# Kernel optimization log

Measured on AMD Instinct MI355X. Metric: run time of the kernel, lower is better.

Reference implementation:

```python
import jax, jax.numpy as jnp
import numpy as np


def channel_attention(x):
    # Faithful to torch: proj_key = x.view(B, -1, C) is a memory RESHAPE, not a transpose.
    B, C, H, W = x.shape
    N = H * W
    pq = x.reshape(B, C, N)          # [B, C, N]
    pk = x.reshape(B, N, C)          # [B, N, C] -- reshape, NOT pq transposed
    attn = jax.nn.softmax(jnp.einsum('bcn,bnd->bcd', pq, pk), axis=-1)  # [B, C, C]
    out = jnp.einsum('bcd,bdn->bcn', attn, pq).reshape(B, C, H, W)
    return out + x


def positional_attention(x):
    B, C, H, W = x.shape
    N = H * W
    pk = x.reshape(B, C, N)                                  # [B, C, N]
    # proj_query = pk transposed -> attn[b, n, m] over spatial positions
    attn = jax.nn.softmax(jnp.einsum('bcn,bcm->bnm', pk, pk), axis=-1)  # [B, N, N]
    # out = bmm(pk, attn^T): out[b, c, m] = sum_n pk[b, c, n] * attn[b, m, n]
    out = jnp.einsum('bcn,bmn->bcm', pk, attn).reshape(B, C, H, W)
    return out + x


def setup_inputs() -> dict:
    key = jax.random.key(0)
    x = jax.random.normal(key, (4, 512, 64, 64), dtype=jnp.float32)
    return {"x": x}


def reference(x):
    x_ca = channel_attention(x)
    x_pa = positional_attention(x_ca)
    return x_pa
```

## Files before the change

kernel.cpp:

```cpp
#include <hip/hip_runtime.h>

#define BATCH 4
#define CH 512
#define NSP 4096

typedef __attribute__((ext_vector_type(8))) short bfrag8;
typedef __attribute__((ext_vector_type(4))) float f32x4;
typedef unsigned short u16;

#define AS1 __attribute__((address_space(1)))
#define AS3 __attribute__((address_space(3)))
__device__ __forceinline__ void gload16(const void* g, void* l) {
    __builtin_amdgcn_global_load_lds((const AS1 void*)g, (AS3 void*)l, 16, 0, 0);
}

__device__ __forceinline__ void split_bf16(float y, u16& h, u16& l) {
    unsigned int u = __float_as_uint(y);
    h = (u16)(u >> 16);
    float r = y - __uint_as_float(((unsigned int)h) << 16);
    l = (u16)(__float_as_uint(r) >> 16);
}
__device__ __forceinline__ float join_bf16(u16 h, u16 l) {
    return __uint_as_float(((unsigned int)h) << 16) + __uint_as_float(((unsigned int)l) << 16);
}

__global__ __launch_bounds__(256) void k_prep_cn(const float* __restrict__ X,
                                                 u16* __restrict__ XHi,
                                                 u16* __restrict__ XLo,
                                                 u16* __restrict__ XT1hi,
                                                 u16* __restrict__ XT1lo) {
    __shared__ unsigned int t[64][65];
    const size_t boff = (size_t)blockIdx.z * CH * NSP;
    const int c0 = blockIdx.y * 64, n0 = blockIdx.x * 64;
    const int r = threadIdx.x >> 4, col4 = (threadIdx.x & 15) * 4;
#pragma unroll
    for (int it = 0; it < 4; it++) {
        int rl = r + it * 16;
        float4 v = *(const float4*)(X + boff + (size_t)(c0 + rl) * NSP + n0 + col4);
        ushort4 h, l;
        split_bf16(v.x, h.x, l.x);
        split_bf16(v.y, h.y, l.y);
        split_bf16(v.z, h.z, l.z);
        split_bf16(v.w, h.w, l.w);
        *(ushort4*)(XHi + boff + (size_t)(c0 + rl) * NSP + n0 + col4) = h;
        *(ushort4*)(XLo + boff + (size_t)(c0 + rl) * NSP + n0 + col4) = l;
        t[rl][col4 + 0] = ((unsigned int)h.x << 16) | l.x;
        t[rl][col4 + 1] = ((unsigned int)h.y << 16) | l.y;
        t[rl][col4 + 2] = ((unsigned int)h.z << 16) | l.z;
        t[rl][col4 + 3] = ((unsigned int)h.w << 16) | l.w;
    }
    __syncthreads();
#pragma unroll
    for (int it = 0; it < 4; it++) {
        int cl = r + it * 16;
        unsigned int p0 = t[col4 + 0][cl];
        unsigned int p1 = t[col4 + 1][cl];
        unsigned int p2 = t[col4 + 2][cl];
        unsigned int p3 = t[col4 + 3][cl];
        ushort4 hv, lv;
        hv.x = p0 >> 16; hv.y = p1 >> 16; hv.z = p2 >> 16; hv.w = p3 >> 16;
        lv.x = p0 & 0xffff; lv.y = p1 & 0xffff; lv.z = p2 & 0xffff; lv.w = p3 & 0xffff;
        *(ushort4*)(XT1hi + boff + (size_t)(n0 + cl) * CH + c0 + col4) = hv;
        *(ushort4*)(XT1lo + boff + (size_t)(n0 + cl) * CH + c0 + col4) = lv;
    }
}

__global__ __launch_bounds__(256) void k_prep_nc(const float* __restrict__ X,
                                                 u16* __restrict__ XT2hi,
                                                 u16* __restrict__ XT2lo) {
    __shared__ unsigned int t[64][65];
    const size_t boff = (size_t)blockIdx.z * CH * NSP;
    const int n0 = blockIdx.x * 64, d0 = blockIdx.y * 64;
    const int r = threadIdx.x >> 4, col4 = (threadIdx.x & 15) * 4;
#pragma unroll
    for (int it = 0; it < 4; it++) {
        int rl = r + it * 16;
        float4 v = *(const float4*)(X + boff + (size_t)(n0 + rl) * CH + d0 + col4);
        ushort4 h, l;
        split_bf16(v.x, h.x, l.x);
        split_bf16(v.y, h.y, l.y);
        split_bf16(v.z, h.z, l.z);
        split_bf16(v.w, h.w, l.w);
        t[rl][col4 + 0] = ((unsigned int)h.x << 16) | l.x;
        t[rl][col4 + 1] = ((unsigned int)h.y << 16) | l.y;
        t[rl][col4 + 2] = ((unsigned int)h.z << 16) | l.z;
        t[rl][col4 + 3] = ((unsigned int)h.w << 16) | l.w;
    }
    __syncthreads();
#pragma unroll
    for (int it = 0; it < 4; it++) {
        int cl = r + it * 16;
        unsigned int p0 = t[col4 + 0][cl];
        unsigned int p1 = t[col4 + 1][cl];
        unsigned int p2 = t[col4 + 2][cl];
        unsigned int p3 = t[col4 + 3][cl];
        ushort4 hv, lv;
        hv.x = p0 >> 16; hv.y = p1 >> 16; hv.z = p2 >> 16; hv.w = p3 >> 16;
        lv.x = p0 & 0xffff; lv.y = p1 & 0xffff; lv.z = p2 & 0xffff; lv.w = p3 & 0xffff;
        *(ushort4*)(XT2hi + boff + (size_t)(d0 + cl) * NSP + n0 + col4) = hv;
        *(ushort4*)(XT2lo + boff + (size_t)(d0 + cl) * NSP + n0 + col4) = lv;
    }
}

__global__ __launch_bounds__(256, 2) void k1_mfma(const u16* __restrict__ XHi,
                                                  const u16* __restrict__ XLo,
                                                  const u16* __restrict__ XT2hi,
                                                  const u16* __restrict__ XT2lo,
                                                  float* __restrict__ Pk) {
    __shared__ __align__(16) char smem[32768];
    char* Ahi = smem;
    char* Alo = smem + 8192;
    char* Bhi = smem + 16384;
    char* Blo = smem + 24576;
    const int bid = blockIdx.x;
    const int xcd = bid & 7;
    const int i1 = bid >> 3;
    const int group = xcd * 4 + (i1 >> 4);
    const int b = group >> 3, kz = group & 7;
    const int tile = i1 & 15;
    const int c0 = (tile >> 2) * 128, d0 = (tile & 3) * 128;
    const size_t boff = (size_t)b * CH * NSP;
    const int tid = threadIdx.x, lane = tid & 63, w = tid >> 6;
    const int wr = w >> 1, wc = w & 1;
    const int rl = lane >> 2;
    const int cb = (lane & 3) * 8;
    f32x4 acc[4][4];
#pragma unroll
    for (int i = 0; i < 4; i++)
#pragma unroll
        for (int j = 0; j < 4; j++) acc[i][j] = (f32x4){0.f, 0.f, 0.f, 0.f};

    const int kbeg = kz * 512, kend = kbeg + 512;
    for (int k0 = kbeg; k0 < kend; k0 += 32) {
#pragma unroll
        for (int s = 0; s < 2; s++) {
            int idx = w * 2 + s;
            int row = 16 * idx + rl;
            gload16(XHi + boff + (size_t)(c0 + row) * NSP + k0 + cb, Ahi + idx * 1024);
            gload16(XLo + boff + (size_t)(c0 + row) * NSP + k0 + cb, Alo + idx * 1024);
            gload16(XT2hi + boff + (size_t)(d0 + row) * NSP + k0 + cb, Bhi + idx * 1024);
            gload16(XT2lo + boff + (size_t)(d0 + row) * NSP + k0 + cb, Blo + idx * 1024);
        }
        __syncthreads();
        bfrag8 ah[4], al[4], bh[4], bl[4];
        const int q16 = (lane >> 4) * 16;
        const int l15 = (lane & 15);
#pragma unroll
        for (int i = 0; i < 4; i++) {
            int offa = (wr * 64 + i * 16 + l15) * 64 + q16;
            ah[i] = *(const bfrag8*)(Ahi + offa);
            al[i] = *(const bfrag8*)(Alo + offa);
            int offb = (wc * 64 + i * 16 + l15) * 64 + q16;
            bh[i] = *(const bfrag8*)(Bhi + offb);
            bl[i] = *(const bfrag8*)(Blo + offb);
        }
#pragma unroll
        for (int i = 0; i < 4; i++)
#pragma unroll
            for (int j = 0; j < 4; j++) {
                acc[i][j] = __builtin_amdgcn_mfma_f32_16x16x32_bf16(ah[i], bh[j], acc[i][j], 0, 0, 0);
                acc[i][j] = __builtin_amdgcn_mfma_f32_16x16x32_bf16(ah[i], bl[j], acc[i][j], 0, 0, 0);
                acc[i][j] = __builtin_amdgcn_mfma_f32_16x16x32_bf16(al[i], bh[j], acc[i][j], 0, 0, 0);
            }
        __syncthreads();
    }
    float* Lb = Pk + (size_t)kz * BATCH * CH * CH + (size_t)b * CH * CH;
    const int col = lane & 15, qr = (lane >> 4) * 4;
#pragma unroll
    for (int i = 0; i < 4; i++)
#pragma unroll
        for (int j = 0; j < 4; j++)
#pragma unroll
            for (int r = 0; r < 4; r++)
                Lb[(size_t)(c0 + wr * 64 + 16 * i + qr + r) * CH + d0 + wc * 64 + 16 * j + col] =
                    acc[i][j][r];
}

__global__ __launch_bounds__(256) void k_combine8(const float* __restrict__ Pk,
                                                  float* __restrict__ Lg) {
    const size_t MM = (size_t)BATCH * CH * CH;
    size_t i = ((size_t)blockIdx.x * 256 + threadIdx.x) * 4;
    float4 s = *(const float4*)(Pk + i);
#pragma unroll
    for (int z = 1; z < 8; z++) {
        float4 v = *(const float4*)(Pk + z * MM + i);
        s.x += v.x; s.y += v.y; s.z += v.z; s.w += v.w;
    }
    *(float4*)(Lg + i) = s;
}

__global__ __launch_bounds__(256) void k_softmax_pack512(float* __restrict__ Lg) {
    __shared__ float buf[512];
    __shared__ float red[256];
    const int tid = threadIdx.x;
    float* row = Lg + (size_t)blockIdx.x * 512;
    float2 v = *(const float2*)(row + tid * 2);
    buf[tid * 2] = v.x;
    buf[tid * 2 + 1] = v.y;
    red[tid] = fmaxf(v.x, v.y);
    __syncthreads();
    for (int s = 128; s > 0; s >>= 1) {
        if (tid < s) red[tid] = fmaxf(red[tid], red[tid + s]);
        __syncthreads();
    }
    float m = red[0];
    __syncthreads();
    float e0 = __expf(buf[tid * 2] - m), e1 = __expf(buf[tid * 2 + 1] - m);
    buf[tid * 2] = e0;
    buf[tid * 2 + 1] = e1;
    red[tid] = e0 + e1;
    __syncthreads();
    for (int s = 128; s > 0; s >>= 1) {
        if (tid < s) red[tid] += red[tid + s];
        __syncthreads();
    }
    float inv = 1.0f / red[0];
    u16* u = (u16*)row;
    u16 h0, l0, h1, l1;
    split_bf16(buf[tid * 2] * inv, h0, l0);
    split_bf16(buf[tid * 2 + 1] * inv, h1, l1);
    __syncthreads();
    u[tid * 2] = h0;
    u[tid * 2 + 1] = h1;
    u[512 + tid * 2] = l0;
    u[512 + tid * 2 + 1] = l1;
}

__global__ __launch_bounds__(256, 2) void k3_mfma(const u16* __restrict__ Lu,
                                                  const u16* __restrict__ XT1hi,
                                                  const u16* __restrict__ XT1lo,
                                                  const float* __restrict__ X,
                                                  u16* __restrict__ Yhi,
                                                  u16* __restrict__ Ylo,
                                                  u16* __restrict__ YThi,
                                                  u16* __restrict__ YTlo) {
    __shared__ __align__(16) char smem[33280];
    char* Ahi = smem;
    char* Alo = smem + 8192;
    char* Bhi = smem + 16384;
    char* Blo = smem + 24576;
    const int b = blockIdx.z;
    const u16* Au = Lu + (size_t)b * CH * 1024;
    const size_t boff = (size_t)b * CH * NSP;
    const float* Xb = X + boff;
    const int tid = threadIdx.x, lane = tid & 63, w = tid >> 6;
    const int wr = w >> 1, wc = w & 1;
    const int c0 = blockIdx.y * 128, n0 = blockIdx.x * 128;
    const int rl = lane >> 2;
    const int cb = (lane & 3) * 8;
    f32x4 acc[4][4];
#pragma unroll
    for (int i = 0; i < 4; i++)
#pragma unroll
        for (int j = 0; j < 4; j++) acc[i][j] = (f32x4){0.f, 0.f, 0.f, 0.f};

    for (int k0 = 0; k0 < CH; k0 += 32) {
#pragma unroll
        for (int s = 0; s < 2; s++) {
            int idx = w * 2 + s;
            int row = 16 * idx + rl;
            gload16(Au + (size_t)(c0 + row) * 1024 + k0 + cb, Ahi + idx * 1024);
            gload16(Au + (size_t)(c0 + row) * 1024 + 512 + k0 + cb, Alo + idx * 1024);
            gload16(XT1hi + boff + (size_t)(n0 + row) * CH + k0 + cb, Bhi + idx * 1024);
            gload16(XT1lo + boff + (size_t)(n0 + row) * CH + k0 + cb, Blo + idx * 1024);
        }
        __syncthreads();
        bfrag8 ah[4], al[4], bh[4], bl[4];
        const int q16 = (lane >> 4) * 16;
        const int l15 = (lane & 15);
#pragma unroll
        for (int i = 0; i < 4; i++) {
            int offa = (wr * 64 + i * 16 + l15) * 64 + q16;
            ah[i] = *(const bfrag8*)(Ahi + offa);
            al[i] = *(const bfrag8*)(Alo + offa);
            int offb = (wc * 64 + i * 16 + l15) * 64 + q16;
            bh[i] = *(const bfrag8*)(Bhi + offb);
            bl[i] = *(const bfrag8*)(Blo + offb);
        }
#pragma unroll
        for (int i = 0; i < 4; i++)
#pragma unroll
            for (int j = 0; j < 4; j++) {
                acc[i][j] = __builtin_amdgcn_mfma_f32_16x16x32_bf16(ah[i], bh[j], acc[i][j], 0, 0, 0);
                acc[i][j] = __builtin_amdgcn_mfma_f32_16x16x32_bf16(ah[i], bl[j], acc[i][j], 0, 0, 0);
                acc[i][j] = __builtin_amdgcn_mfma_f32_16x16x32_bf16(al[i], bh[j], acc[i][j], 0, 0, 0);
            }
        __syncthreads();
    }
    u16* Yhb = Yhi + boff;
    u16* Ylb = Ylo + boff;
    u16* YThb = YThi + boff;
    u16* YTlb = YTlo + boff;
    const int col = lane & 15, qr = (lane >> 4) * 4;
    unsigned int* Tb = (unsigned int*)smem;
#pragma unroll
    for (int round = 0; round < 2; round++) {
        if (wr == round) {
            unsigned int* T = Tb + wc * 4160;
#pragma unroll
            for (int i = 0; i < 4; i++)
#pragma unroll
                for (int j = 0; j < 4; j++)
#pragma unroll
                    for (int r = 0; r < 4; r++) {
                        int cl = 16 * i + qr + r;
                        int nl = 16 * j + col;
                        int c = c0 + wr * 64 + cl;
                        int n = n0 + wc * 64 + nl;
                        float v = acc[i][j][r] + Xb[(size_t)c * NSP + n];
                        u16 h, l;
                        split_bf16(v, h, l);
                        Yhb[(size_t)c * NSP + n] = h;
                        Ylb[(size_t)c * NSP + n] = l;
                        T[nl * 65 + cl] = ((unsigned int)h << 16) | l;
                    }
        }
        __syncthreads();
        if (wr == round) {
            unsigned int* T = Tb + wc * 4160;
            const int cl = (lane & 15) * 4;
#pragma unroll
            for (int rep = 0; rep < 16; rep++) {
                int nq = rep * 4 + (lane >> 4);
                unsigned int p0 = T[nq * 65 + cl];
                unsigned int p1 = T[nq * 65 + cl + 1];
                unsigned int p2 = T[nq * 65 + cl + 2];
                unsigned int p3 = T[nq * 65 + cl + 3];
                ushort4 hv, lv;
                hv.x = p0 >> 16; hv.y = p1 >> 16; hv.z = p2 >> 16; hv.w = p3 >> 16;
                lv.x = p0 & 0xffff; lv.y = p1 & 0xffff; lv.z = p2 & 0xffff; lv.w = p3 & 0xffff;
                size_t o = (size_t)(n0 + wc * 64 + nq) * CH + c0 + wr * 64 + cl;
                *(ushort4*)(YThb + o) = hv;
                *(ushort4*)(YTlb + o) = lv;
            }
        }
        __syncthreads();
    }
}

__global__ __launch_bounds__(256, 2) void k4_mfma(const u16* __restrict__ YThi0,
                                                  const u16* __restrict__ YTlo0,
                                                  float* __restrict__ S0) {
    __shared__ __align__(16) char smem[34816];
    char* Ahi = smem;
    char* Alo = smem + 8192;
    char* Bhi = smem + 16384;
    char* Blo = smem + 24576;
    const int tid = threadIdx.x, lane = tid & 63, w = tid >> 6;
    const int wr = w >> 1, wc = w & 1;
    const int rb = blockIdx.y;
    const u16* YThi = YThi0 + (size_t)rb * NSP * CH;
    const u16* YTlo = YTlo0 + (size_t)rb * NSP * CH;
    float* S = S0 + (size_t)rb * NSP * NSP;
    int idx = blockIdx.x;
    int bi = (int)((sqrtf(8.f * (float)idx + 1.f) - 1.f) * 0.5f);
    while ((bi + 1) * (bi + 2) / 2 <= idx) bi++;
    while (bi * (bi + 1) / 2 > idx) bi--;
    int bj = idx - bi * (bi + 1) / 2;
    const int n0 = bi * 128, m0 = bj * 128;
    const bool diag = (bi == bj);
    const int rl = lane >> 2;
    const int cb = (lane & 3) * 8;
    f32x4 acc[4][4];
#pragma unroll
    for (int i = 0; i < 4; i++)
#pragma unroll
        for (int j = 0; j < 4; j++) acc[i][j] = (f32x4){0.f, 0.f, 0.f, 0.f};

    for (int k0 = 0; k0 < CH; k0 += 32) {
#pragma unroll
        for (int s = 0; s < 2; s++) {
            int i2 = w * 2 + s;
            int row = 16 * i2 + rl;
            gload16(YThi + (size_t)(n0 + row) * CH + k0 + cb, Ahi + i2 * 1024);
            gload16(YTlo + (size_t)(n0 + row) * CH + k0 + cb, Alo + i2 * 1024);
            gload16(YThi + (size_t)(m0 + row) * CH + k0 + cb, Bhi + i2 * 1024);
            gload16(YTlo + (size_t)(m0 + row) * CH + k0 + cb, Blo + i2 * 1024);
        }
        __syncthreads();
        bfrag8 ah[4], al[4], bh[4], bl[4];
        const int q16 = (lane >> 4) * 16;
        const int l15 = (lane & 15);
#pragma unroll
        for (int i = 0; i < 4; i++) {
            int offa = (wr * 64 + i * 16 + l15) * 64 + q16;
            ah[i] = *(const bfrag8*)(Ahi + offa);
            al[i] = *(const bfrag8*)(Alo + offa);
            int offb = (wc * 64 + i * 16 + l15) * 64 + q16;
            bh[i] = *(const bfrag8*)(Bhi + offb);
            bl[i] = *(const bfrag8*)(Blo + offb);
        }
#pragma unroll
        for (int i = 0; i < 4; i++)
#pragma unroll
            for (int j = 0; j < 4; j++) {
                acc[i][j] = __builtin_amdgcn_mfma_f32_16x16x32_bf16(ah[i], bh[j], acc[i][j], 0, 0, 0);
                acc[i][j] = __builtin_amdgcn_mfma_f32_16x16x32_bf16(ah[i], bl[j], acc[i][j], 0, 0, 0);
                acc[i][j] = __builtin_amdgcn_mfma_f32_16x16x32_bf16(al[i], bh[j], acc[i][j], 0, 0, 0);
            }
        __syncthreads();
    }
    const int col = lane & 15, qr = (lane >> 4) * 4;
#pragma unroll
    for (int i = 0; i < 4; i++)
#pragma unroll
        for (int j = 0; j < 4; j++)
#pragma unroll
            for (int r = 0; r < 4; r++)
                S[(size_t)(n0 + wr * 64 + 16 * i + qr + r) * NSP + m0 + wc * 64 + 16 * j + col] =
                    acc[i][j][r];
    if (!diag) {
        float* Tbase = (float*)smem;
#pragma unroll
        for (int round = 0; round < 2; round++) {
            if (wr == round) {
                float* T = Tbase + wc * (64 * 68);
#pragma unroll
                for (int i = 0; i < 4; i++)
#pragma unroll
                    for (int j = 0; j < 4; j++)
#pragma unroll
                        for (int r = 0; r < 4; r++)
                            T[(16 * j + col) * 68 + 16 * i + qr + r] = acc[i][j][r];
            }
            __syncthreads();
            if (wr == round) {
                float* T = Tbase + wc * (64 * 68);
                const int rq = (lane & 15) * 4;
#pragma unroll
                for (int rep = 0; rep < 16; rep++) {
                    int cq = rep * 4 + (lane >> 4);
                    float4 v = *(const float4*)(T + cq * 68 + rq);
                    *(float4*)(S + (size_t)(m0 + wc * 64 + cq) * NSP + n0 + wr * 64 + rq) = v;
                }
            }
            __syncthreads();
        }
    }
}

__global__ __launch_bounds__(256) void k_softmax_pack(float* __restrict__ S) {
    __shared__ float buf[4096];
    __shared__ float red[256];
    const int tid = threadIdx.x;
    float* row = S + (size_t)blockIdx.x * NSP;
    float m = -INFINITY;
#pragma unroll
    for (int it = 0; it < 4; it++) {
        int i = (tid + it * 256) * 4;
        float4 v = *(const float4*)(row + i);
        buf[i] = v.x; buf[i + 1] = v.y; buf[i + 2] = v.z; buf[i + 3] = v.w;
        m = fmaxf(m, fmaxf(fmaxf(v.x, v.y), fmaxf(v.z, v.w)));
    }
    red[tid] = m;
    __syncthreads();
    for (int s = 128; s > 0; s >>= 1) {
        if (tid < s) red[tid] = fmaxf(red[tid], red[tid + s]);
        __syncthreads();
    }
    m = red[0];
    __syncthreads();
    float sum = 0.f;
#pragma unroll
    for (int it = 0; it < 4; it++) {
        int i = (tid + it * 256) * 4;
        float e0 = __expf(buf[i] - m), e1 = __expf(buf[i + 1] - m);
        float e2 = __expf(buf[i + 2] - m), e3 = __expf(buf[i + 3] - m);
        buf[i] = e0; buf[i + 1] = e1; buf[i + 2] = e2; buf[i + 3] = e3;
        sum += e0 + e1 + e2 + e3;
    }
    red[tid] = sum;
    __syncthreads();
    for (int s = 128; s > 0; s >>= 1) {
        if (tid < s) red[tid] += red[tid + s];
        __syncthreads();
    }
    float inv = 1.0f / red[0];
    u16* u = (u16*)row;
#pragma unroll
    for (int it = 0; it < 4; it++) {
        int i = (tid + it * 256) * 4;
        ushort4 hv;
        hv.x = (u16)(__float_as_uint(buf[i] * inv) >> 16);
        hv.y = (u16)(__float_as_uint(buf[i + 1] * inv) >> 16);
        hv.z = (u16)(__float_as_uint(buf[i + 2] * inv) >> 16);
        hv.w = (u16)(__float_as_uint(buf[i + 3] * inv) >> 16);
        *(ushort4*)(u + i) = hv;
    }
}

__global__ __launch_bounds__(256, 2) void k6_mfma(const u16* __restrict__ Yhi0,
                                                  const u16* __restrict__ Ylo0,
                                                  const u16* __restrict__ Su,
                                                  float* __restrict__ Out0,
                                                  float* __restrict__ Pp0,
                                                  float* __restrict__ Pp1) {
    __shared__ __align__(16) char smem[16384];
    char* Ahi = smem;
    char* Bhi = smem + 8192;
    const int tid = threadIdx.x, lane = tid & 63, w = tid >> 6;
    const int wr = w >> 1, wc = w & 1;
    const int m0 = blockIdx.x * 128, c0 = blockIdx.y * 128;
    const int rb = blockIdx.z >> 1, kz = blockIdx.z & 1;
    const u16* Yhi = Yhi0 + (size_t)rb * CH * NSP;
    const u16* Ylo = Ylo0 + (size_t)rb * CH * NSP;
    const u16* Pu = Su + (size_t)rb * NSP * NSP * 2;
    float* Out = Out0 + (size_t)rb * CH * NSP;
    float* Ppart = rb ? Pp1 : Pp0;
    const int kb = kz * 2048;
    const int rl = lane >> 2;
    const int cb = (lane & 3) * 8;
    f32x4 acc[4][4];
#pragma unroll
    for (int i = 0; i < 4; i++)
#pragma unroll
        for (int j = 0; j < 4; j++) acc[i][j] = (f32x4){0.f, 0.f, 0.f, 0.f};

    for (int k0 = 0; k0 < 2048; k0 += 32) {
        const int kk = kb + k0;
#pragma unroll
        for (int s = 0; s < 2; s++) {
            int idx = w * 2 + s;
            int row = 16 * idx + rl;
            gload16(Yhi + (size_t)(c0 + row) * NSP + kk + cb, Ahi + idx * 1024);
            gload16(Pu + (size_t)(m0 + row) * 8192 + kk + cb, Bhi + idx * 1024);
        }
        __syncthreads();
        bfrag8 ah[4], bh[4];
        const int q16 = (lane >> 4) * 16;
        const int l15 = (lane & 15);
#pragma unroll
        for (int i = 0; i < 4; i++) {
            ah[i] = *(const bfrag8*)(Ahi + (wr * 64 + i * 16 + l15) * 64 + q16);
            bh[i] = *(const bfrag8*)(Bhi + (wc * 64 + i * 16 + l15) * 64 + q16);
        }
#pragma unroll
        for (int i = 0; i < 4; i++)
#pragma unroll
            for (int j = 0; j < 4; j++)
                acc[i][j] = __builtin_amdgcn_mfma_f32_16x16x32_bf16(ah[i], bh[j], acc[i][j], 0, 0, 0);
        __syncthreads();
    }
    const int col = lane & 15, qr = (lane >> 4) * 4;
    if (kz == 0) {
#pragma unroll
        for (int i = 0; i < 4; i++)
#pragma unroll
            for (int j = 0; j < 4; j++)
#pragma unroll
                for (int r = 0; r < 4; r++) {
                    int c = c0 + wr * 64 + 16 * i + qr + r;
                    int mm = m0 + wc * 64 + 16 * j + col;
                    Out[(size_t)c * NSP + mm] =
                        acc[i][j][r] +
                        join_bf16(Yhi[(size_t)c * NSP + mm], Ylo[(size_t)c * NSP + mm]);
                }
    } else {
#pragma unroll
        for (int i = 0; i < 4; i++)
#pragma unroll
            for (int j = 0; j < 4; j++)
#pragma unroll
                for (int r = 0; r < 4; r++) {
                    int c = c0 + wr * 64 + 16 * i + qr + r;
                    int mm = m0 + wc * 64 + 16 * j + col;
                    Ppart[(size_t)c * NSP + mm] = acc[i][j][r];
                }
    }
}

__global__ __launch_bounds__(256) void k_fixup(float* __restrict__ Out0,
                                               const float* __restrict__ Pp0,
                                               const float* __restrict__ Pp1) {
    const size_t CN = (size_t)CH * NSP;
    const int b = blockIdx.y;
    const float* P = b ? Pp1 : Pp0;
    float* O = Out0 + (size_t)b * CN;
    size_t i = ((size_t)blockIdx.x * 256 + threadIdx.x) * 4;
    float4 o = *(const float4*)(O + i);
    float4 a = *(const float4*)(P + i);
    o.x += a.x; o.y += a.y; o.z += a.z; o.w += a.w;
    *(float4*)(O + i) = o;
}

extern "C" void kernel_launch(void* const* d_in, const int* in_sizes, int n_in,
                              void* d_out, int out_size, void* d_ws, size_t ws_size,
                              hipStream_t stream) {
    const float* x = (const float*)d_in[0];
    float* out = (float*)d_out;

    char* p = (char*)d_ws;
    const size_t SZ16 = (size_t)BATCH * CH * NSP * 2;
    const size_t HALF = SZ16 / 2;
    u16* XHi = (u16*)p;
    u16* XLo = (u16*)(p + SZ16);
    u16* XT2hi = (u16*)(p + 2 * SZ16);
    u16* XT2lo = (u16*)(p + 3 * SZ16);
    u16* XT1hi = (u16*)(p + 4 * SZ16);
    u16* XT1lo = (u16*)(p + 5 * SZ16);
    float* S = (float*)p;
    u16* Yhi = (u16*)(p + 8 * SZ16);
    u16* Ylo = (u16*)(p + 9 * SZ16);
    u16* YThi = (u16*)(p + 10 * SZ16);
    u16* YTlo = (u16*)(p + 11 * SZ16);
    float* Pk = (float*)(p + 8 * SZ16);
    float* Lg = (float*)(p + 12 * SZ16);

    k_prep_cn<<<dim3(NSP / 64, CH / 64, BATCH), 256, 0, stream>>>(x, XHi, XLo, XT1hi, XT1lo);
    k_prep_nc<<<dim3(NSP / 64, CH / 64, BATCH), 256, 0, stream>>>(x, XT2hi, XT2lo);
    k1_mfma<<<dim3(512), 256, 0, stream>>>(XHi, XLo, XT2hi, XT2lo, Pk);
    k_combine8<<<dim3((BATCH * CH * CH) / (4 * 256)), 256, 0, stream>>>(Pk, Lg);
    k_softmax_pack512<<<dim3(BATCH * CH), 256, 0, stream>>>(Lg);
    k3_mfma<<<dim3(NSP / 128, CH / 128, BATCH), 256, 0, stream>>>((const u16*)Lg, XT1hi, XT1lo, x,
                                                                  Yhi, Ylo, YThi, YTlo);

    const int TRI = (NSP / 128) * (NSP / 128 + 1) / 2;
    for (int round = 0; round < 2; round++) {
        const size_t b0 = (size_t)(2 * round);
        float* Pp0 = (float*)((char*)YThi + round * HALF);
        float* Pp1 = (float*)((char*)YTlo + round * HALF);
        k4_mfma<<<dim3(TRI, 2), 256, 0, stream>>>(YThi + b0 * NSP * CH, YTlo + b0 * NSP * CH, S);
        k_softmax_pack<<<dim3(2 * NSP), 256, 0, stream>>>(S);
        k6_mfma<<<dim3(NSP / 128, CH / 128, 4), 256, 0, stream>>>(Yhi + b0 * CH * NSP,
                                                                  Ylo + b0 * CH * NSP,
                                                                  (const u16*)S,
                                                                  out + b0 * CH * NSP, Pp0, Pp1);
        k_fixup<<<dim3((CH * NSP) / (4 * 256), 2), 256, 0, stream>>>(out + b0 * CH * NSP, Pp0, Pp1);
    }
}
```

Baseline: 504.2 us.

## Rewrite Gram kernel as full-tile 256x256 double-buffered pipeline, dropping symmetry

The positional-attention Gram kernel no longer exploits symmetry with triangular tiles plus a transposed LDS write-back. It now computes every 256x256 tile with 512 threads and an XCD-aware block swizzle. A double-buffered global_load_lds pipeline with explicit vmcnt waits, barriers and setprio overlaps loads with the three split-bf16 MFMA passes. This trades roughly double the MFMA work for removing the transpose epilogue and gaining larger tiles and better latency hiding. It also uses 128KB of LDS per block, which limits occupancy.

```diff
diff --git a/kernel.cpp b/kernel.cpp
--- a/kernel.cpp
+++ b/kernel.cpp
@@ -338,105 +338,132 @@
     }
 }
 
-__global__ __launch_bounds__(256, 2) void k4_mfma(const u16* __restrict__ YThi0,
+__global__ __launch_bounds__(512, 2) void k4_mfma(const u16* __restrict__ YThi0,
                                                   const u16* __restrict__ YTlo0,
                                                   float* __restrict__ S0) {
-    __shared__ __align__(16) char smem[34816];
-    char* Ahi = smem;
-    char* Alo = smem + 8192;
-    char* Bhi = smem + 16384;
-    char* Blo = smem + 24576;
+    __shared__ __align__(16) char smem[131072];
     const int tid = threadIdx.x, lane = tid & 63, w = tid >> 6;
-    const int wr = w >> 1, wc = w & 1;
-    const int rb = blockIdx.y;
-    const u16* YThi = YThi0 + (size_t)rb * NSP * CH;
-    const u16* YTlo = YTlo0 + (size_t)rb * NSP * CH;
+    const int wr = w >> 2, wc = w & 3;
+    const int bid = blockIdx.x;
+    const int swz = (bid & 7) * 64 + (bid >> 3);
+    const int rb = swz >> 8;
+    const int tl = swz & 255;
+    const int n0 = (tl >> 4) * 256, m0 = (tl & 15) * 256;
+    const u16* Phi = YThi0 + (size_t)rb * NSP * CH;
+    const u16* Plo = YTlo0 + (size_t)rb * NSP * CH;
     float* S = S0 + (size_t)rb * NSP * NSP;
-    int idx = blockIdx.x;
-    int bi = (int)((sqrtf(8.f * (float)idx + 1.f) - 1.f) * 0.5f);
-    while ((bi + 1) * (bi + 2) / 2 <= idx) bi++;
-    while (bi * (bi + 1) / 2 > idx) bi--;
-    int bj = idx - bi * (bi + 1) / 2;
-    const int n0 = bi * 128, m0 = bj * 128;
-    const bool diag = (bi == bj);
+
     const int rl = lane >> 2;
     const int cb = (lane & 3) * 8;
-    f32x4 acc[4][4];
-#pragma unroll
-    for (int i = 0; i < 4; i++)
+    const int l15 = lane & 15, q16 = (lane >> 4) * 16;
+
+    auto STAGE = [&](const u16* mat, int r0, int kt, int u) {
+        char* dst = smem + (kt & 1) * 65536 + u * 16384;
+        const int k0 = kt * 32;
+#pragma unroll
+        for (int s = 0; s < 2; s++) {
+            int idx = w * 2 + s;
+            gload16(mat + (size_t)(r0 + idx * 16 + rl) * CH + k0 + cb, dst + idx * 1024);
+        }
+    };
+
+    f32x4 acc[8][4];
+#pragma unroll
+    for (int i = 0; i < 8; i++)
 #pragma unroll
         for (int j = 0; j < 4; j++) acc[i][j] = (f32x4){0.f, 0.f, 0.f, 0.f};
-
-    for (int k0 = 0; k0 < CH; k0 += 32) {
-#pragma unroll
-        for (int s = 0; s < 2; s++) {
-            int i2 = w * 2 + s;
-            int row = 16 * i2 + rl;
-            gload16(YThi + (size_t)(n0 + row) * CH + k0 + cb, Ahi + i2 * 1024);
-            gload16(YTlo + (size_t)(n0 + row) * CH + k0 + cb, Alo + i2 * 1024);
-            gload16(YThi + (size_t)(m0 + row) * CH + k0 + cb, Bhi + i2 * 1024);
-            gload16(YTlo + (size_t)(m0 + row) * CH + k0 + cb, Blo + i2 * 1024);
-        }
-        __syncthreads();
-        bfrag8 ah[4], al[4], bh[4], bl[4];
-        const int q16 = (lane >> 4) * 16;
-        const int l15 = (lane & 15);
-#pragma unroll
-        for (int i = 0; i < 4; i++) {
-            int offa = (wr * 64 + i * 16 + l15) * 64 + q16;
-            ah[i] = *(const bfrag8*)(Ahi + offa);
-            al[i] = *(const bfrag8*)(Alo + offa);
-            int offb = (wc * 64 + i * 16 + l15) * 64 + q16;
-            bh[i] = *(const bfrag8*)(Bhi + offb);
-            bl[i] = *(const bfrag8*)(Blo + offb);
-        }
-#pragma unroll
-        for (int i = 0; i < 4; i++)
-#pragma unroll
-            for (int j = 0; j < 4; j++) {
-                acc[i][j] = __builtin_amdgcn_mfma_f32_16x16x32_bf16(ah[i], bh[j], acc[i][j], 0, 0, 0);
-                acc[i][j] = __builtin_amdgcn_mfma_f32_16x16x32_bf16(ah[i], bl[j], acc[i][j], 0, 0, 0);
-                acc[i][j] = __builtin_amdgcn_mfma_f32_16x16x32_bf16(al[i], bh[j], acc[i][j], 0, 0, 0);
-            }
-        __syncthreads();
-    }
+    bfrag8 ah[8], al[8], bh[4], bl[4];
+
+    auto LDA = [&](const char* base, bfrag8* a) {
+#pragma unroll
+        for (int i = 0; i < 8; i++)
+            a[i] = *(const bfrag8*)(base + (wr * 128 + i * 16 + l15) * 64 + q16);
+    };
+    auto LDB = [&](const char* base, bfrag8* bv) {
+#pragma unroll
+        for (int j = 0; j < 4; j++)
+            bv[j] = *(const bfrag8*)(base + (wc * 64 + j * 16 + l15) * 64 + q16);
+    };
+    auto MMA = [&](const bfrag8* a, const bfrag8* bv) {
+        __builtin_amdgcn_s_setprio(1);
+#pragma unroll
+        for (int i = 0; i < 8; i++)
+#pragma unroll
+            for (int j = 0; j < 4; j++)
+                acc[i][j] = __builtin_amdgcn_mfma_f32_16x16x32_bf16(a[i], bv[j], acc[i][j], 0, 0, 0);
+        __builtin_amdgcn_s_setprio(0);
+        __builtin_amdgcn_s_barrier();
+        __builtin_amdgcn_sched_barrier(0);
+    };
+
+#define WAITB(N)                                          \
+    asm volatile("s_waitcnt vmcnt(" #N ")" ::: "memory"); \
+    __builtin_amdgcn_s_barrier();
+
+    STAGE(Phi, n0, 0, 0);
+    STAGE(Phi, m0, 0, 2);
+    STAGE(Plo, n0, 0, 1);
+    STAGE(Plo, m0, 0, 3);
+    STAGE(Phi, n0, 1, 0);
+    STAGE(Phi, m0, 1, 2);
+    STAGE(Plo, n0, 1, 1);
+    WAITB(10)
+
+    for (int t = 0; t < 14; ++t) {
+        const char* buf = smem + (t & 1) * 65536;
+        LDA(buf, ah);
+        LDB(buf + 32768, bh);
+        STAGE(Plo, m0, t + 1, 3);
+        WAITB(10)
+        MMA(ah, bh);
+        LDA(buf + 16384, al);
+        STAGE(Phi, n0, t + 2, 0);
+        STAGE(Phi, m0, t + 2, 2);
+        WAITB(12)
+        MMA(al, bh);
+        LDB(buf + 49152, bl);
+        STAGE(Plo, n0, t + 2, 1);
+        WAITB(10)
+        MMA(ah, bl);
+    }
+    {
+        const char* buf = smem;
+        LDA(buf, ah);
+        LDB(buf + 32768, bh);
+        STAGE(Plo, m0, 15, 3);
+        WAITB(10)
+        MMA(ah, bh);
+        LDA(buf + 16384, al);
+        WAITB(8)
+        MMA(al, bh);
+        LDB(buf + 49152, bl);
+        WAITB(4)
+        MMA(ah, bl);
+    }
+    {
+        const char* buf = smem + 65536;
+        LDA(buf, ah);
+        LDB(buf + 32768, bh);
+        WAITB(2)
+        MMA(ah, bh);
+        LDA(buf + 16384, al);
+        WAITB(0)
+        MMA(al, bh);
+        LDB(buf + 49152, bl);
+        __builtin_amdgcn_s_barrier();
+        MMA(ah, bl);
+    }
+#undef WAITB
+
     const int col = lane & 15, qr = (lane >> 4) * 4;
 #pragma unroll
-    for (int i = 0; i < 4; i++)
+    for (int i = 0; i < 8; i++)
 #pragma unroll
         for (int j = 0; j < 4; j++)
 #pragma unroll
             for (int r = 0; r < 4; r++)
-                S[(size_t)(n0 + wr * 64 + 16 * i + qr + r) * NSP + m0 + wc * 64 + 16 * j + col] =
+                S[(size_t)(n0 + wr * 128 + 16 * i + qr + r) * NSP + m0 + wc * 64 + 16 * j + col] =
                     acc[i][j][r];
-    if (!diag) {
-        float* Tbase = (float*)smem;
-#pragma unroll
-        for (int round = 0; round < 2; round++) {
-            if (wr == round) {
-                float* T = Tbase + wc * (64 * 68);
-#pragma unroll
-                for (int i = 0; i < 4; i++)
-#pragma unroll
-                    for (int j = 0; j < 4; j++)
-#pragma unroll
-                        for (int r = 0; r < 4; r++)
-                            T[(16 * j + col) * 68 + 16 * i + qr + r] = acc[i][j][r];
-            }
-            __syncthreads();
-            if (wr == round) {
-                float* T = Tbase + wc * (64 * 68);
-                const int rq = (lane & 15) * 4;
-#pragma unroll
-                for (int rep = 0; rep < 16; rep++) {
-                    int cq = rep * 4 + (lane >> 4);
-                    float4 v = *(const float4*)(T + cq * 68 + rq);
-                    *(float4*)(S + (size_t)(m0 + wc * 64 + cq) * NSP + n0 + wr * 64 + rq) = v;
-                }
-            }
-            __syncthreads();
-        }
-    }
 }
 
 __global__ __launch_bounds__(256) void k_softmax_pack(float* __restrict__ S) {
@@ -614,12 +641,11 @@
     k3_mfma<<<dim3(NSP / 128, CH / 128, BATCH), 256, 0, stream>>>((const u16*)Lg, XT1hi, XT1lo, x,
                                                                   Yhi, Ylo, YThi, YTlo);
 
-    const int TRI = (NSP / 128) * (NSP / 128 + 1) / 2;
     for (int round = 0; round < 2; round++) {
         const size_t b0 = (size_t)(2 * round);
         float* Pp0 = (float*)((char*)YThi + round * HALF);
         float* Pp1 = (float*)((char*)YTlo + round * HALF);
-        k4_mfma<<<dim3(TRI, 2), 256, 0, stream>>>(YThi + b0 * NSP * CH, YTlo + b0 * NSP * CH, S);
+        k4_mfma<<<dim3(512), 512, 0, stream>>>(YThi + b0 * NSP * CH, YTlo + b0 * NSP * CH, S);
         k_softmax_pack<<<dim3(2 * NSP), 256, 0, stream>>>(S);
         k6_mfma<<<dim3(NSP / 128, CH / 128, 4), 256, 0, stream>>>(Yhi + b0 * CH * NSP,
                                                                   Ylo + b0 * CH * NSP,
```

Measured after the change: 542.0 us. 1.07x slower.
